# Kernel tuning notes

Measured on AMD Instinct MI355X. Metric: run time of the kernel, lower is better.

## Reference

```python
import jax, jax.numpy as jnp
import numpy as np

B, T, N_EMBD, HEAD = 8, 2048, 1024, 64

def setup_inputs() -> dict:
    key = jax.random.key(0)
    kx, kk, kq, kv = jax.random.split(key, 4)
    x = jax.random.normal(kx, (B, T, N_EMBD), dtype=jnp.float32)
    Wk = jax.random.normal(kk, (HEAD, N_EMBD), dtype=jnp.float32) * 0.02
    Wq = jax.random.normal(kq, (HEAD, N_EMBD), dtype=jnp.float32) * 0.02
    Wv = jax.random.normal(kv, (HEAD, N_EMBD), dtype=jnp.float32) * 0.02
    return {"x": x, "Wk": Wk, "Wq": Wq, "Wv": Wv}

def reference(x, Wk, Wq, Wv):
    # x: [B, T, C]; Linear(n_embd, head_size, bias=False) => x @ W.T
    Bq, Tq, C = x.shape
    q = jnp.einsum('btc,hc->bth', x, Wq)  # [B, T, H]
    k = jnp.einsum('btc,hc->bth', x, Wk)
    v = jnp.einsum('btc,hc->bth', x, Wv)
    # NOTE: source scales by C**0.5 with C = n_embd (not head_size); preserved.
    scale = 1.0 / jnp.sqrt(jnp.float32(C))
    wei = jnp.einsum('bth,bsh->bts', q, k) * scale  # [B, T, T]
    # causal mask: allow key position s <= query position t
    causal = jnp.tril(jnp.ones((Tq, Tq), dtype=bool))
    wei = jnp.where(causal[None, :, :], wei, -jnp.inf)
    wei = jax.nn.softmax(wei, axis=-1)
    # dropout is identity at inference
    out = jnp.einsum('bts,bsh->bth', wei, v)  # [B, T, H]
    return out
```

## Files before the change

### kernel.cpp

```cpp
#include <hip/hip_runtime.h>

#define TB 2048
#define NB 8
#define CEMB 1024
#define HD 64
#define BT (NB*TB)
#define QSCALE 0.04508422f

typedef __attribute__((ext_vector_type(8))) short bf16x8;
typedef __attribute__((ext_vector_type(4))) short bf16x4;
typedef __attribute__((ext_vector_type(4))) float f32x4;

#define MFMA32(a, b, c) __builtin_amdgcn_mfma_f32_16x16x32_bf16(a, b, c, 0, 0, 0)
#define MFMA16(a, b, c) __builtin_amdgcn_mfma_f32_16x16x16bf16_1k(a, b, c, 0, 0, 0)

__device__ inline short f2bf(float f) {
    union { float f; unsigned u; } v; v.f = f;
    unsigned r = v.u + 0x7fffu + ((v.u >> 16) & 1u);
    return (short)(r >> 16);
}
__device__ inline float bf2f(short s) {
    union { unsigned u; float f; } v; v.u = ((unsigned)(unsigned short)s) << 16;
    return v.f;
}
__device__ inline unsigned cvt_pk_bf16(float a, float b) {
    unsigned r;
    asm("v_cvt_pk_bf16_f32 %0, %1, %2" : "=v"(r) : "v"(a), "v"(b));
    return r;
}
__device__ inline bf16x4 pack2(unsigned w0, unsigned w1) {
    union { unsigned u[2]; bf16x4 v; } c; c.u[0] = w0; c.u[1] = w1; return c.v;
}
__device__ inline bf16x8 pack4(unsigned w0, unsigned w1, unsigned w2, unsigned w3) {
    union { unsigned u[4]; bf16x8 v; } c;
    c.u[0] = w0; c.u[1] = w1; c.u[2] = w2; c.u[3] = w3; return c.v;
}
__device__ inline void gload_lds16(const void* g, void* l) {
    __builtin_amdgcn_global_load_lds((const __attribute__((address_space(1))) void*)g,
                                     (__attribute__((address_space(3))) void*)l, 16, 0, 0);
}

__global__ __launch_bounds__(256) void wpack(const float* __restrict__ Wk,
                                             const float* __restrict__ Wq,
                                             const float* __restrict__ Wv,
                                             short* __restrict__ W2) {
    int c = blockIdx.x * 256 + threadIdx.x;
    int lane = c & 63, ntk = c >> 6;
    int nt = ntk % 12, kc = ntk / 12;
    int n = nt * 16 + (lane & 15);
    int col = kc * 32 + (lane >> 4) * 8;
    const float* src = (n < 64) ? Wk + n * 1024
                     : (n < 128) ? Wq + (n - 64) * 1024
                                 : Wv + (n - 128) * 1024;
    float4 a = *(const float4*)(src + col);
    float4 b = *(const float4*)(src + col + 4);
    bf16x8 o;
    o[0] = f2bf(a.x); o[1] = f2bf(a.y); o[2] = f2bf(a.z); o[3] = f2bf(a.w);
    o[4] = f2bf(b.x); o[5] = f2bf(b.y); o[6] = f2bf(b.z); o[7] = f2bf(b.w);
    *(bf16x8*)(W2 + (size_t)c * 8) = o;
}

__global__ __launch_bounds__(512) void qkv_proj(const float* __restrict__ x,
                                                const short* __restrict__ W2,
                                                short* __restrict__ Qb,
                                                short* __restrict__ Kb,
                                                short* __restrict__ Vt) {
    __shared__ __align__(16) char xbuf[3][16384];
    __shared__ __align__(16) char wbuf[3][24576];
    int tid = threadIdx.x, wid = tid >> 6, lane = tid & 63;
    int l15 = lane & 15, quad = lane >> 4;
    int mgrp = wid >> 2;
    int ngrp = wid & 3;
    int m0 = blockIdx.x * 64;

    f32x4 acc[2][3];
#pragma unroll
    for (int i = 0; i < 2; ++i)
#pragma unroll
        for (int j = 0; j < 3; ++j) acc[i][j] = f32x4{0.f, 0.f, 0.f, 0.f};

    int xr0 = wid * 8 + quad;
    int xr1 = wid * 8 + 4 + quad;
    const char* xs0 = (const char*)x + ((size_t)(m0 + xr0) << 12)
                    + ((l15 * 16) ^ ((xr0 & 7) << 4));
    const char* xs1 = (const char*)x + ((size_t)(m0 + xr1) << 12)
                    + ((l15 * 16) ^ ((xr1 & 7) << 4));
    const char* wsrc = (const char*)W2 + (size_t)(wid * 3) * 1024 + lane * 16;

#define STAGE(bsel, t) do { \
        gload_lds16(xs0 + (t) * 256, &xbuf[bsel][wid * 2048]);                      \
        gload_lds16(xs1 + (t) * 256, &xbuf[bsel][wid * 2048 + 1024]);               \
        gload_lds16(wsrc + (size_t)(t) * 24576,        &wbuf[bsel][wid * 3072]);        \
        gload_lds16(wsrc + (size_t)(t) * 24576 + 1024, &wbuf[bsel][wid * 3072 + 1024]); \
        gload_lds16(wsrc + (size_t)(t) * 24576 + 2048, &wbuf[bsel][wid * 3072 + 2048]); } while (0)

    STAGE(0, 0);
    STAGE(1, 1);
    int sw = (l15 & 7) << 4;
#pragma unroll
    for (int t = 0; t < 16; ++t) {
        if (t < 14) {
            STAGE((t + 2) % 3, t + 2);
            asm volatile("s_waitcnt vmcnt(10)" ::: "memory");
        } else if (t == 14) {
            asm volatile("s_waitcnt vmcnt(5)" ::: "memory");
        } else {
            asm volatile("s_waitcnt vmcnt(0)" ::: "memory");
        }
        __builtin_amdgcn_s_barrier();
        __builtin_amdgcn_sched_barrier(0);

        const char* xb = xbuf[t % 3];
        const char* wb = wbuf[t % 3];
        bf16x8 wf[2][3];
        {
            const char* wbn = wb + (size_t)(ngrp * 3) * 1024 + lane * 16;
#pragma unroll
            for (int j = 0; j < 3; ++j) {
                wf[0][j] = *(const bf16x8*)(wbn + j * 1024);
                wf[1][j] = *(const bf16x8*)(wbn + j * 1024 + 12288);
            }
        }
        bf16x8 af[2][2];
#pragma unroll
        for (int mt = 0; mt < 2; ++mt)
#pragma unroll
            for (int kk = 0; kk < 2; ++kk) {
                const char* xr = xb + (mgrp * 32 + mt * 16 + l15) * 256 + kk * 128;
                float4 a0 = *(const float4*)(xr + ((quad * 32) ^ sw));
                float4 a1 = *(const float4*)(xr + ((quad * 32 + 16) ^ sw));
                af[mt][kk] = pack4(cvt_pk_bf16(a0.x, a0.y), cvt_pk_bf16(a0.z, a0.w),
                                   cvt_pk_bf16(a1.x, a1.y), cvt_pk_bf16(a1.z, a1.w));
            }
#pragma unroll
        for (int kk = 0; kk < 2; ++kk)
#pragma unroll
            for (int j = 0; j < 3; ++j) {
                acc[0][j] = MFMA32(af[0][kk], wf[kk][j], acc[0][j]);
                acc[1][j] = MFMA32(af[1][kk], wf[kk][j], acc[1][j]);
            }
        __builtin_amdgcn_s_barrier();
    }
#undef STAGE

    int blk = blockIdx.x;
    int bb = blk >> 5;
    int inb = blk & 31;
#pragma unroll
    for (int j = 0; j < 3; ++j) {
        int gnt = ngrp * 3 + j;
#pragma unroll
        for (int mt = 0; mt < 2; ++mt) {
            int gmt = mgrp * 2 + mt;
            f32x4 s0 = acc[mt][j];
            int row0 = m0 + gmt * 16 + quad * 4;
            if (gnt < 4) {
                int h = gnt * 16 + l15;
#pragma unroll
                for (int r = 0; r < 4; ++r)
                    Kb[(size_t)(row0 + r) * HD + h] = f2bf(s0[r]);
            } else if (gnt < 8) {
                int h = (gnt - 4) * 16 + l15;
#pragma unroll
                for (int r = 0; r < 4; ++r)
                    Qb[(size_t)(row0 + r) * HD + h] = f2bf(s0[r] * QSCALE);
            } else {
                int h = (gnt - 8) * 16 + l15;
                int sblk32 = inb * 2 + (gmt >> 1);
                int half = gmt & 1;
                uint2 v2;
                v2.x = cvt_pk_bf16(s0[0], s0[1]);
                v2.y = cvt_pk_bf16(s0[2], s0[3]);
                *(uint2*)(Vt + ((size_t)((bb * 64 + sblk32) * 64 + h)) * 32
                             + quad * 8 + half * 4) = v2;
            }
        }
    }
}

__global__ __launch_bounds__(256) void flash(const short* __restrict__ Qb,
                                             const short* __restrict__ Kb,
                                             const short* __restrict__ Vt,
                                             float* __restrict__ out) {
    __shared__ float Of[4][2][16][68];
    __shared__ float Ml[4][2][16];
    int tid = threadIdx.x, wave = tid >> 6, lane = tid & 63;
    int l15 = lane & 15, quad = lane >> 4;
    int i = blockIdx.x;
    int round = i >> 8, s = i & 255;
    int b = s & 7;
    int g32 = s >> 3;
    int q32 = round ? 63 - g32 : g32;
    int tq0 = q32 * 32;
    size_t bT = (size_t)b * TB;

    const short* qr0 = Qb + (bT + tq0 + l15) * HD;
    const short* qr1 = Qb + (bT + tq0 + 16 + l15) * HD;
    bf16x8 qf00 = *(const bf16x8*)(qr0 + quad * 8);
    bf16x8 qf01 = *(const bf16x8*)(qr0 + 32 + quad * 8);
    bf16x8 qf10 = *(const bf16x8*)(qr1 + quad * 8);
    bf16x8 qf11 = *(const bf16x8*)(qr1 + 32 + quad * 8);

    bf16x4 ones4;
#pragma unroll
    for (int j = 0; j < 4; ++j) ones4[j] = (short)0x3F80;

    f32x4 accO0[4], accO1[4];
#pragma unroll
    for (int k = 0; k < 4; ++k) { accO0[k] = f32x4{0.f,0.f,0.f,0.f}; accO1[k] = f32x4{0.f,0.f,0.f,0.f}; }
    f32x4 accL0 = f32x4{0.f,0.f,0.f,0.f}, accL1 = f32x4{0.f,0.f,0.f,0.f};

    int ntiles = (tq0 + 95) >> 6;
    const short* kbase = Kb + bT * HD;
    const short* vtb = Vt + (size_t)b * 131072;

    int myt = wave;
    if (myt < ntiles) {
        bf16x8 kf[8];
        {
            const short* kr = kbase + (size_t)(myt * 64 + l15) * HD + quad * 8;
#pragma unroll
            for (int st = 0; st < 4; ++st) {
                kf[st * 2]     = *(const bf16x8*)(kr + (size_t)st * 16 * HD);
                kf[st * 2 + 1] = *(const bf16x8*)(kr + (size_t)st * 16 * HD + 32);
            }
        }
        for (; myt < ntiles; myt += 4) {
            int s0 = myt * 64;
            bf16x8 vf8[8];
#pragma unroll
            for (int sb2 = 0; sb2 < 2; ++sb2)
#pragma unroll
                for (int ht = 0; ht < 4; ++ht)
                    vf8[sb2 * 4 + ht] = *(const bf16x8*)(
                        vtb + ((size_t)(((s0 >> 5) + sb2) * 64 + ht * 16 + l15)) * 32 + quad * 8);
            f32x4 sv0[4], sv1[4];
            __builtin_amdgcn_s_setprio(1);
#pragma unroll
            for (int st = 0; st < 4; ++st) {
                f32x4 t0 = f32x4{0.f,0.f,0.f,0.f}, t1 = f32x4{0.f,0.f,0.f,0.f};
                t0 = MFMA32(kf[st * 2], qf00, t0);
                t0 = MFMA32(kf[st * 2 + 1], qf01, t0);
                t1 = MFMA32(kf[st * 2], qf10, t1);
                t1 = MFMA32(kf[st * 2 + 1], qf11, t1);
                sv0[st] = t0; sv1[st] = t1;
            }
            __builtin_amdgcn_s_setprio(0);
            if (myt + 4 < ntiles) {
                const short* kr = kbase + (size_t)(s0 + 256 + l15) * HD + quad * 8;
#pragma unroll
                for (int st = 0; st < 4; ++st) {
                    kf[st * 2]     = *(const bf16x8*)(kr + (size_t)st * 16 * HD);
                    kf[st * 2 + 1] = *(const bf16x8*)(kr + (size_t)st * 16 * HD + 32);
                }
            }
            bf16x4 pk0[4], pk1[4];
            if (s0 + 63 <= tq0) {
#pragma unroll
                for (int st = 0; st < 4; ++st) {
                    unsigned w00 = cvt_pk_bf16(__builtin_amdgcn_exp2f(sv0[st][0]),
                                               __builtin_amdgcn_exp2f(sv0[st][1]));
                    unsigned w01 = cvt_pk_bf16(__builtin_amdgcn_exp2f(sv0[st][2]),
                                               __builtin_amdgcn_exp2f(sv0[st][3]));
                    unsigned w10 = cvt_pk_bf16(__builtin_amdgcn_exp2f(sv1[st][0]),
                                               __builtin_amdgcn_exp2f(sv1[st][1]));
                    unsigned w11 = cvt_pk_bf16(__builtin_amdgcn_exp2f(sv1[st][2]),
                                               __builtin_amdgcn_exp2f(sv1[st][3]));
                    pk0[st] = pack2(w00, w01);
                    pk1[st] = pack2(w10, w11);
                }
            } else {
                int t0g = tq0 + l15, t1g = tq0 + 16 + l15;
#pragma unroll
                for (int st = 0; st < 4; ++st) {
                    bool full0 = (s0 + st * 16 + 15 <= tq0);
                    bool full1 = (s0 + st * 16 + 15 <= tq0 + 16);
                    int sb = s0 + st * 16 + quad * 4;
                    float a0 = (full0 || sb + 0 <= t0g) ? __builtin_amdgcn_exp2f(sv0[st][0]) : 0.f;
                    float a1 = (full0 || sb + 1 <= t0g) ? __builtin_amdgcn_exp2f(sv0[st][1]) : 0.f;
                    float a2 = (full0 || sb + 2 <= t0g) ? __builtin_amdgcn_exp2f(sv0[st][2]) : 0.f;
                    float a3 = (full0 || sb + 3 <= t0g) ? __builtin_amdgcn_exp2f(sv0[st][3]) : 0.f;
                    float c0 = (full1 || sb + 0 <= t1g) ? __builtin_amdgcn_exp2f(sv1[st][0]) : 0.f;
                    float c1 = (full1 || sb + 1 <= t1g) ? __builtin_amdgcn_exp2f(sv1[st][1]) : 0.f;
                    float c2 = (full1 || sb + 2 <= t1g) ? __builtin_amdgcn_exp2f(sv1[st][2]) : 0.f;
                    float c3 = (full1 || sb + 3 <= t1g) ? __builtin_amdgcn_exp2f(sv1[st][3]) : 0.f;
                    pk0[st] = pack2(cvt_pk_bf16(a0, a1), cvt_pk_bf16(a2, a3));
                    pk1[st] = pack2(cvt_pk_bf16(c0, c1), cvt_pk_bf16(c2, c3));
                }
            }
            __builtin_amdgcn_s_setprio(1);
#pragma unroll
            for (int g = 0; g < 4; ++g) {
                accL0 = MFMA16(ones4, pk0[g], accL0);
                accL1 = MFMA16(ones4, pk1[g], accL1);
#pragma unroll
                for (int ht = 0; ht < 4; ++ht) {
                    bf16x8 v = vf8[(g >> 1) * 4 + ht];
                    bf16x4 va;
                    if (g & 1) { va[0] = v[4]; va[1] = v[5]; va[2] = v[6]; va[3] = v[7]; }
                    else       { va[0] = v[0]; va[1] = v[1]; va[2] = v[2]; va[3] = v[3]; }
                    accO0[ht] = MFMA16(va, pk0[g], accO0[ht]);
                    accO1[ht] = MFMA16(va, pk1[g], accO1[ht]);
                }
            }
            __builtin_amdgcn_s_setprio(0);
        }
    }

#pragma unroll
    for (int ht = 0; ht < 4; ++ht) {
        float4 o0, o1;
        o0.x = accO0[ht][0]; o0.y = accO0[ht][1]; o0.z = accO0[ht][2]; o0.w = accO0[ht][3];
        o1.x = accO1[ht][0]; o1.y = accO1[ht][1]; o1.z = accO1[ht][2]; o1.w = accO1[ht][3];
        *(float4*)&Of[wave][0][l15][ht * 16 + quad * 4] = o0;
        *(float4*)&Of[wave][1][l15][ht * 16 + quad * 4] = o1;
    }
    if (quad == 0) { Ml[wave][0][l15] = accL0[0]; Ml[wave][1][l15] = accL1[0]; }
    __syncthreads();

    int row = tid >> 4, c4 = (tid & 15) * 4;
#pragma unroll
    for (int qt = 0; qt < 2; ++qt) {
        float L = Ml[0][qt][row] + Ml[1][qt][row] + Ml[2][qt][row] + Ml[3][qt][row];
        float inv = 1.0f / L;
        float4 p0 = *(const float4*)&Of[0][qt][row][c4];
        float4 p1 = *(const float4*)&Of[1][qt][row][c4];
        float4 p2 = *(const float4*)&Of[2][qt][row][c4];
        float4 p3 = *(const float4*)&Of[3][qt][row][c4];
        float4 o;
        o.x = (p0.x + p1.x + p2.x + p3.x) * inv;
        o.y = (p0.y + p1.y + p2.y + p3.y) * inv;
        o.z = (p0.z + p1.z + p2.z + p3.z) * inv;
        o.w = (p0.w + p1.w + p2.w + p3.w) * inv;
        *(float4*)(out + (bT + tq0 + qt * 16 + row) * HD + c4) = o;
    }
}

extern "C" void kernel_launch(void* const* d_in, const int* in_sizes, int n_in,
                              void* d_out, int out_size, void* d_ws, size_t ws_size,
                              hipStream_t stream) {
    const float* x  = (const float*)d_in[0];
    const float* Wk = (const float*)d_in[1];
    const float* Wq = (const float*)d_in[2];
    const float* Wv = (const float*)d_in[3];
    float* out = (float*)d_out;

    short* W2 = (short*)d_ws;
    short* Qb = W2 + 192 * 1024;
    short* Kb = Qb + (size_t)BT * HD;
    short* Vt = Kb + (size_t)BT * HD;

    wpack<<<96, 256, 0, stream>>>(Wk, Wq, Wv, W2);
    qkv_proj<<<256, 512, 0, stream>>>(x, W2, Qb, Kb, Vt);
    flash<<<512, 256, 0, stream>>>(Qb, Kb, Vt, out);
}
```

Baseline: 131.5 us.

## Pre-cast x to bf16 in a separate kernel and load A fragments directly

Adds an xcast kernel that converts the fp32 activations to bf16 in workspace. The projection kernel then reads bf16 A fragments straight from global memory into registers with a three-deep register prefetch, and only the weights are staged through double-buffered LDS. This removes the per-tile fp32 LDS staging and in-loop conversion from the matmul, and halves its activation read volume. The cost is an extra kernel launch and an extra full pass over x (read fp32, write bf16, read back), so total memory traffic for x roughly doubles. The path also needs enough workspace to hold the bf16 copy of x.

Result: slower. 142.1 us (+8.1%).

```diff
diff --git a/kernel.cpp b/kernel.cpp
--- a/kernel.cpp
+++ b/kernel.cpp
@@ -60,13 +60,26 @@
     *(bf16x8*)(W2 + (size_t)c * 8) = o;
 }
 
-__global__ __launch_bounds__(512) void qkv_proj(const float* __restrict__ x,
-                                                const short* __restrict__ W2,
-                                                short* __restrict__ Qb,
-                                                short* __restrict__ Kb,
-                                                short* __restrict__ Vt) {
-    __shared__ __align__(16) char xbuf[3][16384];
-    __shared__ __align__(16) char wbuf[3][24576];
+__global__ __launch_bounds__(256) void xcast(const float* __restrict__ x,
+                                             short* __restrict__ xb) {
+    int i = blockIdx.x * 256 + threadIdx.x;
+#pragma unroll 4
+    for (int g = i; g < (BT * CEMB / 8); g += 2048 * 256) {
+        const float4* src = (const float4*)(x + (size_t)g * 8);
+        float4 a = src[0], b = src[1];
+        uint4 o;
+        o.x = cvt_pk_bf16(a.x, a.y); o.y = cvt_pk_bf16(a.z, a.w);
+        o.z = cvt_pk_bf16(b.x, b.y); o.w = cvt_pk_bf16(b.z, b.w);
+        *(uint4*)(xb + (size_t)g * 8) = o;
+    }
+}
+
+__global__ __launch_bounds__(512) void qkv_mm(const short* __restrict__ xb,
+                                              const short* __restrict__ W2,
+                                              short* __restrict__ Qb,
+                                              short* __restrict__ Kb,
+                                              short* __restrict__ Vt) {
+    __shared__ __align__(16) char wbuf[2][24576];
     int tid = threadIdx.x, wid = tid >> 6, lane = tid & 63;
     int l15 = lane & 15, quad = lane >> 4;
     int mgrp = wid >> 2;
@@ -79,69 +92,50 @@
 #pragma unroll
         for (int j = 0; j < 3; ++j) acc[i][j] = f32x4{0.f, 0.f, 0.f, 0.f};
 
-    int xr0 = wid * 8 + quad;
-    int xr1 = wid * 8 + 4 + quad;
-    const char* xs0 = (const char*)x + ((size_t)(m0 + xr0) << 12)
-                    + ((l15 * 16) ^ ((xr0 & 7) << 4));
-    const char* xs1 = (const char*)x + ((size_t)(m0 + xr1) << 12)
-                    + ((l15 * 16) ^ ((xr1 & 7) << 4));
-    const char* wsrc = (const char*)W2 + (size_t)(wid * 3) * 1024 + lane * 16;
-
-#define STAGE(bsel, t) do { \
-        gload_lds16(xs0 + (t) * 256, &xbuf[bsel][wid * 2048]);                      \
-        gload_lds16(xs1 + (t) * 256, &xbuf[bsel][wid * 2048 + 1024]);               \
+    const char* wsrc = (const char*)W2 + wid * 3072 + lane * 16;
+    const char* arow0 = (const char*)xb + (size_t)(m0 + mgrp * 32 + l15) * 2048 + quad * 16;
+    const char* arow1 = arow0 + 16 * 2048;
+
+    bf16x8 abuf[3][4];
+
+#define WSTAGE(bsel, t) do { \
         gload_lds16(wsrc + (size_t)(t) * 24576,        &wbuf[bsel][wid * 3072]);        \
         gload_lds16(wsrc + (size_t)(t) * 24576 + 1024, &wbuf[bsel][wid * 3072 + 1024]); \
         gload_lds16(wsrc + (size_t)(t) * 24576 + 2048, &wbuf[bsel][wid * 3072 + 2048]); } while (0)
-
-    STAGE(0, 0);
-    STAGE(1, 1);
-    int sw = (l15 & 7) << 4;
+#define ALOAD(t) do { \
+        abuf[(t) % 3][0] = *(const bf16x8*)(arow0 + (t) * 128);      \
+        abuf[(t) % 3][1] = *(const bf16x8*)(arow0 + (t) * 128 + 64); \
+        abuf[(t) % 3][2] = *(const bf16x8*)(arow1 + (t) * 128);      \
+        abuf[(t) % 3][3] = *(const bf16x8*)(arow1 + (t) * 128 + 64); } while (0)
+
+    WSTAGE(0, 0);
+    __builtin_amdgcn_sched_barrier(0);
+    ALOAD(0); ALOAD(1);
 #pragma unroll
     for (int t = 0; t < 16; ++t) {
-        if (t < 14) {
-            STAGE((t + 2) % 3, t + 2);
-            asm volatile("s_waitcnt vmcnt(10)" ::: "memory");
-        } else if (t == 14) {
-            asm volatile("s_waitcnt vmcnt(5)" ::: "memory");
-        } else {
-            asm volatile("s_waitcnt vmcnt(0)" ::: "memory");
+        if (t + 1 < 16) WSTAGE((t + 1) & 1, t + 1);
+        __builtin_amdgcn_sched_barrier(0);
+        if (t + 2 < 16) ALOAD(t + 2);
+        if (t <= 13)      asm volatile("s_waitcnt vmcnt(11)" ::: "memory");
+        else if (t == 14) asm volatile("s_waitcnt vmcnt(7)"  ::: "memory");
+        else              asm volatile("s_waitcnt vmcnt(0)"  ::: "memory");
+        __builtin_amdgcn_s_barrier();
+        __builtin_amdgcn_sched_barrier(0);
+
+        const char* wbn = &wbuf[t & 1][ngrp * 3072 + lane * 16];
+#pragma unroll
+        for (int j = 0; j < 3; ++j) {
+            bf16x8 wf0 = *(const bf16x8*)(wbn + j * 1024);
+            bf16x8 wf1 = *(const bf16x8*)(wbn + j * 1024 + 12288);
+            acc[0][j] = MFMA32(abuf[t % 3][0], wf0, acc[0][j]);
+            acc[0][j] = MFMA32(abuf[t % 3][1], wf1, acc[0][j]);
+            acc[1][j] = MFMA32(abuf[t % 3][2], wf0, acc[1][j]);
+            acc[1][j] = MFMA32(abuf[t % 3][3], wf1, acc[1][j]);
         }
         __builtin_amdgcn_s_barrier();
-        __builtin_amdgcn_sched_barrier(0);
-
-        const char* xb = xbuf[t % 3];
-        const char* wb = wbuf[t % 3];
-        bf16x8 wf[2][3];
-        {
-            const char* wbn = wb + (size_t)(ngrp * 3) * 1024 + lane * 16;
-#pragma unroll
-            for (int j = 0; j < 3; ++j) {
-                wf[0][j] = *(const bf16x8*)(wbn + j * 1024);
-                wf[1][j] = *(const bf16x8*)(wbn + j * 1024 + 12288);
-            }
-        }
-        bf16x8 af[2][2];
-#pragma unroll
-        for (int mt = 0; mt < 2; ++mt)
-#pragma unroll
-            for (int kk = 0; kk < 2; ++kk) {
-                const char* xr = xb + (mgrp * 32 + mt * 16 + l15) * 256 + kk * 128;
-                float4 a0 = *(const float4*)(xr + ((quad * 32) ^ sw));
-                float4 a1 = *(const float4*)(xr + ((quad * 32 + 16) ^ sw));
-                af[mt][kk] = pack4(cvt_pk_bf16(a0.x, a0.y), cvt_pk_bf16(a0.z, a0.w),
-                                   cvt_pk_bf16(a1.x, a1.y), cvt_pk_bf16(a1.z, a1.w));
-            }
-#pragma unroll
-        for (int kk = 0; kk < 2; ++kk)
-#pragma unroll
-            for (int j = 0; j < 3; ++j) {
-                acc[0][j] = MFMA32(af[0][kk], wf[kk][j], acc[0][j]);
-                acc[1][j] = MFMA32(af[1][kk], wf[kk][j], acc[1][j]);
-            }
-        __builtin_amdgcn_s_barrier();
-    }
-#undef STAGE
+    }
+#undef WSTAGE
+#undef ALOAD
 
     int blk = blockIdx.x;
     int bb = blk >> 5;
@@ -349,8 +343,10 @@
     short* Qb = W2 + 192 * 1024;
     short* Kb = Qb + (size_t)BT * HD;
     short* Vt = Kb + (size_t)BT * HD;
+    short* xb = Vt + (size_t)NB * 64 * 64 * 32;
 
     wpack<<<96, 256, 0, stream>>>(Wk, Wq, Wv, W2);
-    qkv_proj<<<256, 512, 0, stream>>>(x, W2, Qb, Kb, Vt);
+    xcast<<<2048, 256, 0, stream>>>(x, xb);
+    qkv_mm<<<256, 512, 0, stream>>>(xb, W2, Qb, Kb, Vt);
     flash<<<512, 256, 0, stream>>>(Qb, Kb, Vt, out);
 }
```

## Fuse weight pack, QKV projection and flash attention into one persistent kernel

Applied to the files above, without the earlier changes.

Replaces the three kernel launches with a single 512-block kernel that uses a global atomic barrier between the phases: weight packing, QKV projection and causal attention. The projection is retiled to 32 rows per block with double buffering so that all 512 blocks take part, and blocks that are idle during weight packing prefetch their slice of x into cache. The goal is to remove launch gaps and tail effects between kernels. In exchange it needs all 512 blocks to be co-resident, since the spin barrier deadlocks otherwise, and it adds a memset plus barrier latency.

Result: slower. 369.3 us (+180.9%).

```diff
diff --git a/kernel.cpp b/kernel.cpp
--- a/kernel.cpp
+++ b/kernel.cpp
@@ -19,10 +19,6 @@
     unsigned r = v.u + 0x7fffu + ((v.u >> 16) & 1u);
     return (short)(r >> 16);
 }
-__device__ inline float bf2f(short s) {
-    union { unsigned u; float f; } v; v.u = ((unsigned)(unsigned short)s) << 16;
-    return v.f;
-}
 __device__ inline unsigned cvt_pk_bf16(float a, float b) {
     unsigned r;
     asm("v_cvt_pk_bf16_f32 %0, %1, %2" : "=v"(r) : "v"(a), "v"(b));
@@ -40,120 +36,119 @@
                                      (__attribute__((address_space(3))) void*)l, 16, 0, 0);
 }
 
-__global__ __launch_bounds__(256) void wpack(const float* __restrict__ Wk,
-                                             const float* __restrict__ Wq,
-                                             const float* __restrict__ Wv,
-                                             short* __restrict__ W2) {
-    int c = blockIdx.x * 256 + threadIdx.x;
-    int lane = c & 63, ntk = c >> 6;
-    int nt = ntk % 12, kc = ntk / 12;
-    int n = nt * 16 + (lane & 15);
-    int col = kc * 32 + (lane >> 4) * 8;
-    const float* src = (n < 64) ? Wk + n * 1024
-                     : (n < 128) ? Wq + (n - 64) * 1024
-                                 : Wv + (n - 128) * 1024;
-    float4 a = *(const float4*)(src + col);
-    float4 b = *(const float4*)(src + col + 4);
-    bf16x8 o;
-    o[0] = f2bf(a.x); o[1] = f2bf(a.y); o[2] = f2bf(a.z); o[3] = f2bf(a.w);
-    o[4] = f2bf(b.x); o[5] = f2bf(b.y); o[6] = f2bf(b.z); o[7] = f2bf(b.w);
-    *(bf16x8*)(W2 + (size_t)c * 8) = o;
-}
-
-__global__ __launch_bounds__(512) void qkv_proj(const float* __restrict__ x,
-                                                const short* __restrict__ W2,
+__device__ inline void gsync(unsigned* bar, unsigned nb) {
+    __syncthreads();
+    if (threadIdx.x == 0) {
+        __threadfence();
+        unsigned old = __hip_atomic_fetch_add(bar, 1u, __ATOMIC_ACQ_REL,
+                                              __HIP_MEMORY_SCOPE_AGENT);
+        unsigned tgt = (old / nb + 1u) * nb;
+        while (__hip_atomic_load(bar, __ATOMIC_ACQUIRE, __HIP_MEMORY_SCOPE_AGENT) < tgt)
+            __builtin_amdgcn_s_sleep(2);
+    }
+    __syncthreads();
+    __threadfence();
+}
+
+union SMem {
+    struct { char xb[2][4096]; char wb[2][12288]; } q;
+    struct { float Of[4][2][16][68]; float Ml[4][2][16]; } f;
+};
+
+__global__ __launch_bounds__(256, 3) void fused(const float* __restrict__ x,
+                                                const float* __restrict__ Wk,
+                                                const float* __restrict__ Wq,
+                                                const float* __restrict__ Wv,
+                                                short* __restrict__ W2,
                                                 short* __restrict__ Qb,
                                                 short* __restrict__ Kb,
-                                                short* __restrict__ Vt) {
-    __shared__ __align__(16) char xbuf[3][16384];
-    __shared__ __align__(16) char wbuf[3][24576];
-    int tid = threadIdx.x, wid = tid >> 6, lane = tid & 63;
-    int l15 = lane & 15, quad = lane >> 4;
-    int mgrp = wid >> 2;
-    int ngrp = wid & 3;
-    int m0 = blockIdx.x * 64;
-
-    f32x4 acc[2][3];
-#pragma unroll
-    for (int i = 0; i < 2; ++i)
-#pragma unroll
-        for (int j = 0; j < 3; ++j) acc[i][j] = f32x4{0.f, 0.f, 0.f, 0.f};
-
-    int xr0 = wid * 8 + quad;
-    int xr1 = wid * 8 + 4 + quad;
-    const char* xs0 = (const char*)x + ((size_t)(m0 + xr0) << 12)
-                    + ((l15 * 16) ^ ((xr0 & 7) << 4));
-    const char* xs1 = (const char*)x + ((size_t)(m0 + xr1) << 12)
-                    + ((l15 * 16) ^ ((xr1 & 7) << 4));
-    const char* wsrc = (const char*)W2 + (size_t)(wid * 3) * 1024 + lane * 16;
-
-#define STAGE(bsel, t) do { \
-        gload_lds16(xs0 + (t) * 256, &xbuf[bsel][wid * 2048]);                      \
-        gload_lds16(xs1 + (t) * 256, &xbuf[bsel][wid * 2048 + 1024]);               \
-        gload_lds16(wsrc + (size_t)(t) * 24576,        &wbuf[bsel][wid * 3072]);        \
-        gload_lds16(wsrc + (size_t)(t) * 24576 + 1024, &wbuf[bsel][wid * 3072 + 1024]); \
-        gload_lds16(wsrc + (size_t)(t) * 24576 + 2048, &wbuf[bsel][wid * 3072 + 2048]); } while (0)
-
-    STAGE(0, 0);
-    STAGE(1, 1);
-    int sw = (l15 & 7) << 4;
-#pragma unroll
-    for (int t = 0; t < 16; ++t) {
-        if (t < 14) {
-            STAGE((t + 2) % 3, t + 2);
-            asm volatile("s_waitcnt vmcnt(10)" ::: "memory");
-        } else if (t == 14) {
-            asm volatile("s_waitcnt vmcnt(5)" ::: "memory");
-        } else {
-            asm volatile("s_waitcnt vmcnt(0)" ::: "memory");
-        }
-        __builtin_amdgcn_s_barrier();
-        __builtin_amdgcn_sched_barrier(0);
-
-        const char* xb = xbuf[t % 3];
-        const char* wb = wbuf[t % 3];
-        bf16x8 wf[2][3];
-        {
-            const char* wbn = wb + (size_t)(ngrp * 3) * 1024 + lane * 16;
-#pragma unroll
-            for (int j = 0; j < 3; ++j) {
-                wf[0][j] = *(const bf16x8*)(wbn + j * 1024);
-                wf[1][j] = *(const bf16x8*)(wbn + j * 1024 + 12288);
-            }
-        }
-        bf16x8 af[2][2];
-#pragma unroll
-        for (int mt = 0; mt < 2; ++mt)
-#pragma unroll
-            for (int kk = 0; kk < 2; ++kk) {
-                const char* xr = xb + (mgrp * 32 + mt * 16 + l15) * 256 + kk * 128;
-                float4 a0 = *(const float4*)(xr + ((quad * 32) ^ sw));
-                float4 a1 = *(const float4*)(xr + ((quad * 32 + 16) ^ sw));
-                af[mt][kk] = pack4(cvt_pk_bf16(a0.x, a0.y), cvt_pk_bf16(a0.z, a0.w),
-                                   cvt_pk_bf16(a1.x, a1.y), cvt_pk_bf16(a1.z, a1.w));
-            }
-#pragma unroll
-        for (int kk = 0; kk < 2; ++kk)
-#pragma unroll
-            for (int j = 0; j < 3; ++j) {
-                acc[0][j] = MFMA32(af[0][kk], wf[kk][j], acc[0][j]);
-                acc[1][j] = MFMA32(af[1][kk], wf[kk][j], acc[1][j]);
-            }
-        __builtin_amdgcn_s_barrier();
+                                                short* __restrict__ Vt,
+                                                float* __restrict__ out,
+                                                unsigned* __restrict__ bar) {
+    __shared__ __align__(16) SMem sm;
+    int tid = threadIdx.x;
+
+    if (blockIdx.x < 96) {
+        int c = blockIdx.x * 256 + tid;
+        int lane = c & 63, ntk = c >> 6;
+        int nt = ntk % 12, kc = ntk / 12;
+        int n = nt * 16 + (lane & 15);
+        int col = kc * 32 + (lane >> 4) * 8;
+        const float* src = (n < 64) ? Wk + n * 1024
+                         : (n < 128) ? Wq + (n - 64) * 1024
+                                     : Wv + (n - 128) * 1024;
+        float4 a = *(const float4*)(src + col);
+        float4 b = *(const float4*)(src + col + 4);
+        bf16x8 o;
+        o[0] = f2bf(a.x); o[1] = f2bf(a.y); o[2] = f2bf(a.z); o[3] = f2bf(a.w);
+        o[4] = f2bf(b.x); o[5] = f2bf(b.y); o[6] = f2bf(b.z); o[7] = f2bf(b.w);
+        *(bf16x8*)(W2 + (size_t)c * 8) = o;
+    } else {
+        const float* xp = x + (size_t)blockIdx.x * 32 * CEMB;
+        float s = 0.f;
+#pragma unroll
+        for (int k = 0; k < 8; ++k) s += xp[tid * 16 + k * 4096];
+        asm volatile("" :: "v"(s));
     }
-#undef STAGE
-
-    int blk = blockIdx.x;
-    int bb = blk >> 5;
-    int inb = blk & 31;
-#pragma unroll
-    for (int j = 0; j < 3; ++j) {
-        int gnt = ngrp * 3 + j;
-#pragma unroll
-        for (int mt = 0; mt < 2; ++mt) {
-            int gmt = mgrp * 2 + mt;
-            f32x4 s0 = acc[mt][j];
-            int row0 = m0 + gmt * 16 + quad * 4;
+    gsync(bar, 512);
+
+    {
+        int wid = tid >> 6, lane = tid & 63;
+        int l15 = lane & 15, quad = lane >> 4;
+        int mgrp = wid >> 1, ngrp = wid & 1;
+        int m0 = blockIdx.x * 32;
+
+        f32x4 acc[6];
+#pragma unroll
+        for (int j = 0; j < 6; ++j) acc[j] = f32x4{0.f, 0.f, 0.f, 0.f};
+
+        int rl = lane >> 3;
+        const char* xsrc = (const char*)x + ((size_t)(m0 + wid * 8 + rl) << 12)
+                         + (((lane & 7) * 16) ^ ((rl & 7) << 4));
+        const char* wsrc = (const char*)W2 + (size_t)(wid * 3) * 1024 + lane * 16;
+
+#define STG(bsel, t) do { \
+        gload_lds16(wsrc + (size_t)(t) * 12288,        &sm.q.wb[bsel][wid * 3072]);        \
+        gload_lds16(wsrc + (size_t)(t) * 12288 + 1024, &sm.q.wb[bsel][wid * 3072 + 1024]); \
+        gload_lds16(wsrc + (size_t)(t) * 12288 + 2048, &sm.q.wb[bsel][wid * 3072 + 2048]); \
+        gload_lds16(xsrc + (t) * 128, &sm.q.xb[bsel][wid * 1024]); } while (0)
+
+        STG(0, 0);
+        int arow = mgrp * 16 + l15;
+        int sca = (quad * 32)      ^ ((arow & 7) << 4);
+        int scb = (quad * 32 + 16) ^ ((arow & 7) << 4);
+        const char* wn0 = (const char*)&sm.q.wb[0][0] + (size_t)(ngrp * 6) * 1024 + lane * 16;
+
+        for (int t = 0; t < 32; ++t) {
+            if (t < 31) {
+                STG((t + 1) & 1, t + 1);
+                asm volatile("s_waitcnt vmcnt(4)" ::: "memory");
+            } else {
+                asm volatile("s_waitcnt vmcnt(0)" ::: "memory");
+            }
+            __builtin_amdgcn_s_barrier();
+
+            const char* xbp = &sm.q.xb[t & 1][0];
+            const char* wn  = wn0 + (t & 1) * 12288;
+            float4 a0 = *(const float4*)(xbp + arow * 128 + sca);
+            float4 a1 = *(const float4*)(xbp + arow * 128 + scb);
+            bf16x8 af = pack4(cvt_pk_bf16(a0.x, a0.y), cvt_pk_bf16(a0.z, a0.w),
+                              cvt_pk_bf16(a1.x, a1.y), cvt_pk_bf16(a1.z, a1.w));
+#pragma unroll
+            for (int j = 0; j < 6; ++j) {
+                bf16x8 wf = *(const bf16x8*)(wn + j * 1024);
+                acc[j] = MFMA32(af, wf, acc[j]);
+            }
+            __builtin_amdgcn_s_barrier();
+        }
+#undef STG
+
+        int bb = blockIdx.x >> 6, sblk32 = blockIdx.x & 63;
+#pragma unroll
+        for (int j = 0; j < 6; ++j) {
+            int gnt = ngrp * 6 + j;
+            f32x4 s0 = acc[j];
+            int row0 = m0 + mgrp * 16 + quad * 4;
             if (gnt < 4) {
                 int h = gnt * 16 + l15;
 #pragma unroll
@@ -166,173 +161,167 @@
                     Qb[(size_t)(row0 + r) * HD + h] = f2bf(s0[r] * QSCALE);
             } else {
                 int h = (gnt - 8) * 16 + l15;
-                int sblk32 = inb * 2 + (gmt >> 1);
-                int half = gmt & 1;
                 uint2 v2;
                 v2.x = cvt_pk_bf16(s0[0], s0[1]);
                 v2.y = cvt_pk_bf16(s0[2], s0[3]);
                 *(uint2*)(Vt + ((size_t)((bb * 64 + sblk32) * 64 + h)) * 32
-                             + quad * 8 + half * 4) = v2;
+                             + quad * 8 + mgrp * 4) = v2;
             }
         }
     }
-}
-
-__global__ __launch_bounds__(256) void flash(const short* __restrict__ Qb,
-                                             const short* __restrict__ Kb,
-                                             const short* __restrict__ Vt,
-                                             float* __restrict__ out) {
-    __shared__ float Of[4][2][16][68];
-    __shared__ float Ml[4][2][16];
-    int tid = threadIdx.x, wave = tid >> 6, lane = tid & 63;
-    int l15 = lane & 15, quad = lane >> 4;
-    int i = blockIdx.x;
-    int round = i >> 8, s = i & 255;
-    int b = s & 7;
-    int g32 = s >> 3;
-    int q32 = round ? 63 - g32 : g32;
-    int tq0 = q32 * 32;
-    size_t bT = (size_t)b * TB;
-
-    const short* qr0 = Qb + (bT + tq0 + l15) * HD;
-    const short* qr1 = Qb + (bT + tq0 + 16 + l15) * HD;
-    bf16x8 qf00 = *(const bf16x8*)(qr0 + quad * 8);
-    bf16x8 qf01 = *(const bf16x8*)(qr0 + 32 + quad * 8);
-    bf16x8 qf10 = *(const bf16x8*)(qr1 + quad * 8);
-    bf16x8 qf11 = *(const bf16x8*)(qr1 + 32 + quad * 8);
-
-    bf16x4 ones4;
-#pragma unroll
-    for (int j = 0; j < 4; ++j) ones4[j] = (short)0x3F80;
-
-    f32x4 accO0[4], accO1[4];
-#pragma unroll
-    for (int k = 0; k < 4; ++k) { accO0[k] = f32x4{0.f,0.f,0.f,0.f}; accO1[k] = f32x4{0.f,0.f,0.f,0.f}; }
-    f32x4 accL0 = f32x4{0.f,0.f,0.f,0.f}, accL1 = f32x4{0.f,0.f,0.f,0.f};
-
-    int ntiles = (tq0 + 95) >> 6;
-    const short* kbase = Kb + bT * HD;
-    const short* vtb = Vt + (size_t)b * 131072;
-
-    int myt = wave;
-    if (myt < ntiles) {
-        bf16x8 kf[8];
-        {
-            const short* kr = kbase + (size_t)(myt * 64 + l15) * HD + quad * 8;
-#pragma unroll
-            for (int st = 0; st < 4; ++st) {
-                kf[st * 2]     = *(const bf16x8*)(kr + (size_t)st * 16 * HD);
-                kf[st * 2 + 1] = *(const bf16x8*)(kr + (size_t)st * 16 * HD + 32);
-            }
-        }
-        for (; myt < ntiles; myt += 4) {
-            int s0 = myt * 64;
-            bf16x8 vf8[8];
-#pragma unroll
-            for (int sb2 = 0; sb2 < 2; ++sb2)
-#pragma unroll
-                for (int ht = 0; ht < 4; ++ht)
-                    vf8[sb2 * 4 + ht] = *(const bf16x8*)(
-                        vtb + ((size_t)(((s0 >> 5) + sb2) * 64 + ht * 16 + l15)) * 32 + quad * 8);
-            f32x4 sv0[4], sv1[4];
-            __builtin_amdgcn_s_setprio(1);
-#pragma unroll
-            for (int st = 0; st < 4; ++st) {
-                f32x4 t0 = f32x4{0.f,0.f,0.f,0.f}, t1 = f32x4{0.f,0.f,0.f,0.f};
-                t0 = MFMA32(kf[st * 2], qf00, t0);
-                t0 = MFMA32(kf[st * 2 + 1], qf01, t0);
-                t1 = MFMA32(kf[st * 2], qf10, t1);
-                t1 = MFMA32(kf[st * 2 + 1], qf11, t1);
-                sv0[st] = t0; sv1[st] = t1;
-            }
-            __builtin_amdgcn_s_setprio(0);
-            if (myt + 4 < ntiles) {
-                const short* kr = kbase + (size_t)(s0 + 256 + l15) * HD + quad * 8;
+    gsync(bar, 512);
+
+    {
+        int wave = tid >> 6, lane = tid & 63;
+        int l15 = lane & 15, quad = lane >> 4;
+        int i = blockIdx.x;
+        int round = i >> 8, s = i & 255;
+        int b = s & 7;
+        int g32 = s >> 3;
+        int q32 = round ? 63 - g32 : g32;
+        int tq0 = q32 * 32;
+        size_t bT = (size_t)b * TB;
+
+        const short* qr0 = Qb + (bT + tq0 + l15) * HD;
+        const short* qr1 = Qb + (bT + tq0 + 16 + l15) * HD;
+        bf16x8 qf00 = *(const bf16x8*)(qr0 + quad * 8);
+        bf16x8 qf01 = *(const bf16x8*)(qr0 + 32 + quad * 8);
+        bf16x8 qf10 = *(const bf16x8*)(qr1 + quad * 8);
+        bf16x8 qf11 = *(const bf16x8*)(qr1 + 32 + quad * 8);
+
+        bf16x4 ones4;
+#pragma unroll
+        for (int j = 0; j < 4; ++j) ones4[j] = (short)0x3F80;
+
+        f32x4 accO0[4], accO1[4];
+#pragma unroll
+        for (int k = 0; k < 4; ++k) { accO0[k] = f32x4{0.f,0.f,0.f,0.f}; accO1[k] = f32x4{0.f,0.f,0.f,0.f}; }
+        f32x4 accL0 = f32x4{0.f,0.f,0.f,0.f}, accL1 = f32x4{0.f,0.f,0.f,0.f};
+
+        int ntiles = (tq0 + 95) >> 6;
+        const short* kbase = Kb + bT * HD;
+        const short* vtb = Vt + (size_t)b * 131072;
+
+        int myt = wave;
+        if (myt < ntiles) {
+            bf16x8 kf[8];
+            {
+                const short* kr = kbase + (size_t)(myt * 64 + l15) * HD + quad * 8;
 #pragma unroll
                 for (int st = 0; st < 4; ++st) {
                     kf[st * 2]     = *(const bf16x8*)(kr + (size_t)st * 16 * HD);
                     kf[st * 2 + 1] = *(const bf16x8*)(kr + (size_t)st * 16 * HD + 32);
                 }
             }
-            bf16x4 pk0[4], pk1[4];
-            if (s0 + 63 <= tq0) {
+            for (; myt < ntiles; myt += 4) {
+                int s0 = myt * 64;
+                bf16x8 vf8[8];
+#pragma unroll
+                for (int sb2 = 0; sb2 < 2; ++sb2)
+#pragma unroll
+                    for (int ht = 0; ht < 4; ++ht)
+                        vf8[sb2 * 4 + ht] = *(const bf16x8*)(
+                            vtb + ((size_t)(((s0 >> 5) + sb2) * 64 + ht * 16 + l15)) * 32 + quad * 8);
+                f32x4 sv0[4], sv1[4];
+                __builtin_amdgcn_s_setprio(1);
 #pragma unroll
                 for (int st = 0; st < 4; ++st) {
-                    unsigned w00 = cvt_pk_bf16(__builtin_amdgcn_exp2f(sv0[st][0]),
-                                               __builtin_amdgcn_exp2f(sv0[st][1]));
-                    unsigned w01 = cvt_pk_bf16(__builtin_amdgcn_exp2f(sv0[st][2]),
-                                               __builtin_amdgcn_exp2f(sv0[st][3]));
-                    unsigned w10 = cvt_pk_bf16(__builtin_amdgcn_exp2f(sv1[st][0]),
-                                               __builtin_amdgcn_exp2f(sv1[st][1]));
-                    unsigned w11 = cvt_pk_bf16(__builtin_amdgcn_exp2f(sv1[st][2]),
-                                               __builtin_amdgcn_exp2f(sv1[st][3]));
-                    pk0[st] = pack2(w00, w01);
-                    pk1[st] = pack2(w10, w11);
-                }
-            } else {
-                int t0g = tq0 + l15, t1g = tq0 + 16 + l15;
-#pragma unroll
-                for (int st = 0; st < 4; ++st) {
-                    bool full0 = (s0 + st * 16 + 15 <= tq0);
-                    bool full1 = (s0 + st * 16 + 15 <= tq0 + 16);
-                    int sb = s0 + st * 16 + quad * 4;
-                    float a0 = (full0 || sb + 0 <= t0g) ? __builtin_amdgcn_exp2f(sv0[st][0]) : 0.f;
-                    float a1 = (full0 || sb + 1 <= t0g) ? __builtin_amdgcn_exp2f(sv0[st][1]) : 0.f;
-                    float a2 = (full0 || sb + 2 <= t0g) ? __builtin_amdgcn_exp2f(sv0[st][2]) : 0.f;
-                    float a3 = (full0 || sb + 3 <= t0g) ? __builtin_amdgcn_exp2f(sv0[st][3]) : 0.f;
-                    float c0 = (full1 || sb + 0 <= t1g) ? __builtin_amdgcn_exp2f(sv1[st][0]) : 0.f;
-                    float c1 = (full1 || sb + 1 <= t1g) ? __builtin_amdgcn_exp2f(sv1[st][1]) : 0.f;
-                    float c2 = (full1 || sb + 2 <= t1g) ? __builtin_amdgcn_exp2f(sv1[st][2]) : 0.f;
-                    float c3 = (full1 || sb + 3 <= t1g) ? __builtin_amdgcn_exp2f(sv1[st][3]) : 0.f;
-                    pk0[st] = pack2(cvt_pk_bf16(a0, a1), cvt_pk_bf16(a2, a3));
-                    pk1[st] = pack2(cvt_pk_bf16(c0, c1), cvt_pk_bf16(c2, c3));
-                }
-            }
-            __builtin_amdgcn_s_setprio(1);
-#pragma unroll
-            for (int g = 0; g < 4; ++g) {
-                accL0 = MFMA16(ones4, pk0[g], accL0);
-                accL1 = MFMA16(ones4, pk1[g], accL1);
-#pragma unroll
-                for (int ht = 0; ht < 4; ++ht) {
-                    bf16x8 v = vf8[(g >> 1) * 4 + ht];
-                    bf16x4 va;
-                    if (g & 1) { va[0] = v[4]; va[1] = v[5]; va[2] = v[6]; va[3] = v[7]; }
-                    else       { va[0] = v[0]; va[1] = v[1]; va[2] = v[2]; va[3] = v[3]; }
-                    accO0[ht] = MFMA16(va, pk0[g], accO0[ht]);
-                    accO1[ht] = MFMA16(va, pk1[g], accO1[ht]);
-                }
-            }
-            __builtin_amdgcn_s_setprio(0);
-        }
-    }
-
-#pragma unroll
-    for (int ht = 0; ht < 4; ++ht) {
-        float4 o0, o1;
-        o0.x = accO0[ht][0]; o0.y = accO0[ht][1]; o0.z = accO0[ht][2]; o0.w = accO0[ht][3];
-        o1.x = accO1[ht][0]; o1.y = accO1[ht][1]; o1.z = accO1[ht][2]; o1.w = accO1[ht][3];
-        *(float4*)&Of[wave][0][l15][ht * 16 + quad * 4] = o0;
-        *(float4*)&Of[wave][1][l15][ht * 16 + quad * 4] = o1;
-    }
-    if (quad == 0) { Ml[wave][0][l15] = accL0[0]; Ml[wave][1][l15] = accL1[0]; }
-    __syncthreads();
-
-    int row = tid >> 4, c4 = (tid & 15) * 4;
-#pragma unroll
-    for (int qt = 0; qt < 2; ++qt) {
-        float L = Ml[0][qt][row] + Ml[1][qt][row] + Ml[2][qt][row] + Ml[3][qt][row];
-        float inv = 1.0f / L;
-        float4 p0 = *(const float4*)&Of[0][qt][row][c4];
-        float4 p1 = *(const float4*)&Of[1][qt][row][c4];
-        float4 p2 = *(const float4*)&Of[2][qt][row][c4];
-        float4 p3 = *(const float4*)&Of[3][qt][row][c4];
-        float4 o;
-        o.x = (p0.x + p1.x + p2.x + p3.x) * inv;
-        o.y = (p0.y + p1.y + p2.y + p3.y) * inv;
-        o.z = (p0.z + p1.z + p2.z + p3.z) * inv;
-        o.w = (p0.w + p1.w + p2.w + p3.w) * inv;
-        *(float4*)(out + (bT + tq0 + qt * 16 + row) * HD + c4) = o;
+                    f32x4 t0 = f32x4{0.f,0.f,0.f,0.f}, t1 = f32x4{0.f,0.f,0.f,0.f};
+                    t0 = MFMA32(kf[st * 2], qf00, t0);
+                    t0 = MFMA32(kf[st * 2 + 1], qf01, t0);
+                    t1 = MFMA32(kf[st * 2], qf10, t1);
+                    t1 = MFMA32(kf[st * 2 + 1], qf11, t1);
+                    sv0[st] = t0; sv1[st] = t1;
+                }
+                __builtin_amdgcn_s_setprio(0);
+                if (myt + 4 < ntiles) {
+                    const short* kr = kbase + (size_t)(s0 + 256 + l15) * HD + quad * 8;
+#pragma unroll
+                    for (int st = 0; st < 4; ++st) {
+                        kf[st * 2]     = *(const bf16x8*)(kr + (size_t)st * 16 * HD);
+                        kf[st * 2 + 1] = *(const bf16x8*)(kr + (size_t)st * 16 * HD + 32);
+                    }
+                }
+                bf16x4 pk0[4], pk1[4];
+                if (s0 + 63 <= tq0) {
+#pragma unroll
+                    for (int st = 0; st < 4; ++st) {
+                        unsigned w00 = cvt_pk_bf16(__builtin_amdgcn_exp2f(sv0[st][0]),
+                                                   __builtin_amdgcn_exp2f(sv0[st][1]));
+                        unsigned w01 = cvt_pk_bf16(__builtin_amdgcn_exp2f(sv0[st][2]),
+                                                   __builtin_amdgcn_exp2f(sv0[st][3]));
+                        unsigned w10 = cvt_pk_bf16(__builtin_amdgcn_exp2f(sv1[st][0]),
+                                                   __builtin_amdgcn_exp2f(sv1[st][1]));
+                        unsigned w11 = cvt_pk_bf16(__builtin_amdgcn_exp2f(sv1[st][2]),
+                                                   __builtin_amdgcn_exp2f(sv1[st][3]));
+                        pk0[st] = pack2(w00, w01);
+                        pk1[st] = pack2(w10, w11);
+                    }
+                } else {
+                    int t0g = tq0 + l15, t1g = tq0 + 16 + l15;
+#pragma unroll
+                    for (int st = 0; st < 4; ++st) {
+                        bool full0 = (s0 + st * 16 + 15 <= tq0);
+                        bool full1 = (s0 + st * 16 + 15 <= tq0 + 16);
+                        int sb = s0 + st * 16 + quad * 4;
+                        float a0 = (full0 || sb + 0 <= t0g) ? __builtin_amdgcn_exp2f(sv0[st][0]) : 0.f;
+                        float a1 = (full0 || sb + 1 <= t0g) ? __builtin_amdgcn_exp2f(sv0[st][1]) : 0.f;
+                        float a2 = (full0 || sb + 2 <= t0g) ? __builtin_amdgcn_exp2f(sv0[st][2]) : 0.f;
+                        float a3 = (full0 || sb + 3 <= t0g) ? __builtin_amdgcn_exp2f(sv0[st][3]) : 0.f;
+                        float c0 = (full1 || sb + 0 <= t1g) ? __builtin_amdgcn_exp2f(sv1[st][0]) : 0.f;
+                        float c1 = (full1 || sb + 1 <= t1g) ? __builtin_amdgcn_exp2f(sv1[st][1]) : 0.f;
+                        float c2 = (full1 || sb + 2 <= t1g) ? __builtin_amdgcn_exp2f(sv1[st][2]) : 0.f;
+                        float c3 = (full1 || sb + 3 <= t1g) ? __builtin_amdgcn_exp2f(sv1[st][3]) : 0.f;
+                        pk0[st] = pack2(cvt_pk_bf16(a0, a1), cvt_pk_bf16(a2, a3));
+                        pk1[st] = pack2(cvt_pk_bf16(c0, c1), cvt_pk_bf16(c2, c3));
+                    }
+                }
+                __builtin_amdgcn_s_setprio(1);
+#pragma unroll
+                for (int g = 0; g < 4; ++g) {
+                    accL0 = MFMA16(ones4, pk0[g], accL0);
+                    accL1 = MFMA16(ones4, pk1[g], accL1);
+#pragma unroll
+                    for (int ht = 0; ht < 4; ++ht) {
+                        bf16x8 v = vf8[(g >> 1) * 4 + ht];
+                        bf16x4 va;
+                        if (g & 1) { va[0] = v[4]; va[1] = v[5]; va[2] = v[6]; va[3] = v[7]; }
+                        else       { va[0] = v[0]; va[1] = v[1]; va[2] = v[2]; va[3] = v[3]; }
+                        accO0[ht] = MFMA16(va, pk0[g], accO0[ht]);
+                        accO1[ht] = MFMA16(va, pk1[g], accO1[ht]);
+                    }
+                }
+                __builtin_amdgcn_s_setprio(0);
+            }
+        }
+
+#pragma unroll
+        for (int ht = 0; ht < 4; ++ht) {
+            float4 o0, o1;
+            o0.x = accO0[ht][0]; o0.y = accO0[ht][1]; o0.z = accO0[ht][2]; o0.w = accO0[ht][3];
+            o1.x = accO1[ht][0]; o1.y = accO1[ht][1]; o1.z = accO1[ht][2]; o1.w = accO1[ht][3];
+            *(float4*)&sm.f.Of[wave][0][l15][ht * 16 + quad * 4] = o0;
+            *(float4*)&sm.f.Of[wave][1][l15][ht * 16 + quad * 4] = o1;
+        }
+        if (quad == 0) { sm.f.Ml[wave][0][l15] = accL0[0]; sm.f.Ml[wave][1][l15] = accL1[0]; }
+        __syncthreads();
+
+        int row = tid >> 4, c4 = (tid & 15) * 4;
+#pragma unroll
+        for (int qt = 0; qt < 2; ++qt) {
+            float L = sm.f.Ml[0][qt][row] + sm.f.Ml[1][qt][row] + sm.f.Ml[2][qt][row] + sm.f.Ml[3][qt][row];
+            float inv = 1.0f / L;
+            float4 p0 = *(const float4*)&sm.f.Of[0][qt][row][c4];
+            float4 p1 = *(const float4*)&sm.f.Of[1][qt][row][c4];
+            float4 p2 = *(const float4*)&sm.f.Of[2][qt][row][c4];
+            float4 p3 = *(const float4*)&sm.f.Of[3][qt][row][c4];
+            float4 o;
+            o.x = (p0.x + p1.x + p2.x + p3.x) * inv;
+            o.y = (p0.y + p1.y + p2.y + p3.y) * inv;
+            o.z = (p0.z + p1.z + p2.z + p3.z) * inv;
+            o.w = (p0.w + p1.w + p2.w + p3.w) * inv;
+            *(float4*)(out + (bT + tq0 + qt * 16 + row) * HD + c4) = o;
+        }
     }
 }
 
@@ -349,8 +338,8 @@
     short* Qb = W2 + 192 * 1024;
     short* Kb = Qb + (size_t)BT * HD;
     short* Vt = Kb + (size_t)BT * HD;
-
-    wpack<<<96, 256, 0, stream>>>(Wk, Wq, Wv, W2);
-    qkv_proj<<<256, 512, 0, stream>>>(x, W2, Qb, Kb, Vt);
-    flash<<<512, 256, 0, stream>>>(Qb, Kb, Vt, out);
-}
+    unsigned* bar = (unsigned*)((char*)d_ws + (16u << 20));
+
+    hipMemsetAsync(bar, 0, 16, stream);
+    fused<<<512, 256, 0, stream>>>(x, Wk, Wq, Wv, W2, Qb, Kb, Vt, out, bar);
+}
```
